# Kernel tuning notes

Measured on AMD Instinct MI355X. Metric: run time of the kernel, lower is better.

## Reference

```python
import jax, jax.numpy as jnp
import numpy as np

N_NODES = 100000


def _deg_isqrt(idx, n):
    # clamped-to-1 degree, then ^-0.5 (DGL GraphConv norm='both')
    deg = jax.ops.segment_sum(jnp.ones(idx.shape, jnp.float32), idx, num_segments=n)
    return jnp.power(jnp.maximum(deg, 1.0), -0.5)


def _graph_conv(feat, W, b, src, dst, out_isqrt, in_isqrt, n):
    # norm='both': scale by src out-degree^-1/2, mult-first (in>out), spmm, scale by dst in-degree^-1/2
    h = (feat * out_isqrt[:, None]) @ W                      # [N, out]
    h = jax.ops.segment_sum(h[src], dst, num_segments=n)     # gather/scatter over edges
    return h * in_isqrt[:, None] + b


def setup_inputs() -> dict:
    key = jax.random.key(0)
    ks = jax.random.split(key, 10)
    in_dim, h1, h2 = 512, 64, 32
    n, e = N_NODES, 800000
    features = jax.random.normal(ks[0], (n, in_dim), jnp.float32)
    src = jax.random.randint(ks[1], (e,), 0, n)
    dst = jax.random.randint(ks[2], (e,), 0, n)
    noise = jax.random.normal(ks[3], (n, h2), jnp.float32)
    s1 = 1.0 / np.sqrt(in_dim)
    s2 = 1.0 / np.sqrt(h1)
    W1 = jax.random.uniform(ks[4], (in_dim, h1), jnp.float32, -s1, s1)
    b1 = jnp.zeros((h1,), jnp.float32)
    W2 = jax.random.uniform(ks[5], (h1, h2), jnp.float32, -s2, s2)
    b2 = jnp.zeros((h2,), jnp.float32)
    W3 = jax.random.uniform(ks[6], (h1, h2), jnp.float32, -s2, s2)
    b3 = jnp.zeros((h2,), jnp.float32)
    return {"features": features, "src": src, "dst": dst, "noise": noise,
            "W1": W1, "b1": b1, "W2": W2, "b2": b2, "W3": W3, "b3": b3}


def reference(features, src, dst, noise, W1, b1, W2, b2, W3, b3):
    n = features.shape[0]
    out_isqrt = _deg_isqrt(src, n)
    in_isqrt = _deg_isqrt(dst, n)
    h = jax.nn.relu(_graph_conv(features, W1, b1, src, dst, out_isqrt, in_isqrt, n))
    mean = _graph_conv(h, W2, b2, src, dst, out_isqrt, in_isqrt, n)
    log_std = _graph_conv(h, W3, b3, src, dst, out_isqrt, in_isqrt, n)
    z = mean + noise * jnp.exp(log_std)
    return z, mean, log_std
```

## Files before the change

### kernel.cpp

```cpp
#include <hip/hip_runtime.h>
#include <hip/hip_bf16.h>


typedef __attribute__((ext_vector_type(8))) short short8;
typedef __attribute__((ext_vector_type(4))) float f32x4;
typedef unsigned short ushort_t;

static __device__ inline short f2bf(float f)
{
    union { __hip_bfloat16 h; short s; } u;
    u.h = __float2bfloat16(f);
    return u.s;
}

static __device__ inline float bf2f(ushort_t u)
{
    union { float f; unsigned v; } w;
    w.v = ((unsigned)u) << 16;
    return w.f;
}

static __device__ inline short8 cvt8(float4 lo, float4 hi)
{
    short8 r;
    r[0] = f2bf(lo.x); r[1] = f2bf(lo.y); r[2] = f2bf(lo.z); r[3] = f2bf(lo.w);
    r[4] = f2bf(hi.x); r[5] = f2bf(hi.y); r[6] = f2bf(hi.z); r[7] = f2bf(hi.w);
    return r;
}

__global__ __launch_bounds__(256) void k_setup(
    const float* __restrict__ W1, const float* __restrict__ W2,
    const float* __restrict__ W3, short* __restrict__ w1f,
    float* __restrict__ wc, int4* __restrict__ zp, int z4)
{
    int gid = blockIdx.x * 256 + threadIdx.x;
    if (gid < z4) zp[gid] = make_int4(0, 0, 0, 0);
    if (gid < 64 * 64) {
        int k = gid >> 6, c = gid & 63;
        wc[gid] = (c < 32) ? W2[k * 32 + c] : W3[k * 32 + (c - 32)];
    }
    if (gid < 512 * 64) {
        int k = gid >> 6, c = gid & 63;
        int kt = k >> 5, kk = k & 31, nt = c >> 4, lr = c & 15;
        int kg = kk >> 3, j = kk & 7;
        int l = kg * 16 + lr;
        w1f[(kt * 4 + nt) * 512 + l * 8 + j] = f2bf(W1[gid]);
    }
}

__global__ __launch_bounds__(256) void k_deg_int(
    const int* __restrict__ src, const int* __restrict__ dst,
    int* __restrict__ degS, int* __restrict__ degD, int e)
{
    int gid = blockIdx.x * 256 + threadIdx.x;
    if (gid >= e) return;
    atomicAdd(&degS[src[gid]], 1);
    atomicAdd(&degD[dst[gid]], 1);
}

__global__ __launch_bounds__(256) void k_scan_block_sums(
    const int* __restrict__ deg, int* __restrict__ partials, int n)
{
    __shared__ int red[256];
    int gid = blockIdx.x * 256 + threadIdx.x;
    red[threadIdx.x] = (gid < n) ? deg[gid] : 0;
    __syncthreads();
    for (int s = 128; s > 0; s >>= 1) {
        if (threadIdx.x < s) red[threadIdx.x] += red[threadIdx.x + s];
        __syncthreads();
    }
    if (threadIdx.x == 0) partials[blockIdx.x] = red[0];
}

__global__ __launch_bounds__(512) void k_scan_partials(
    int* __restrict__ partials, int nb)
{
    __shared__ int s[512];
    int t = threadIdx.x;
    s[t] = (t < nb) ? partials[t] : 0;
    __syncthreads();
    for (int d = 1; d < 512; d <<= 1) {
        int v = (t >= d) ? s[t - d] : 0;
        __syncthreads();
        s[t] += v;
        __syncthreads();
    }
    if (t < nb) partials[t] = (t == 0) ? 0 : s[t - 1];
}

__global__ __launch_bounds__(256) void k_scan_final(
    const int* __restrict__ degD, const int* __restrict__ degS,
    const int* __restrict__ partials,
    int* __restrict__ row_ptr, int* __restrict__ cursor,
    float* __restrict__ isq_out, float* __restrict__ isq_in, int n)
{
    __shared__ int s[256];
    int t = threadIdx.x;
    int gid = blockIdx.x * 256 + t;
    int v = (gid < n) ? degD[gid] : 0;
    s[t] = v;
    __syncthreads();
    for (int d = 1; d < 256; d <<= 1) {
        int u = (t >= d) ? s[t - d] : 0;
        __syncthreads();
        s[t] += u;
        __syncthreads();
    }
    int start = partials[blockIdx.x] + s[t] - v;
    if (gid < n) {
        row_ptr[gid] = start;
        cursor[gid]  = start;
        isq_in[gid]  = 1.0f / sqrtf((float)max(v, 1));
        isq_out[gid] = 1.0f / sqrtf((float)max(degS[gid], 1));
    }
    if (gid == n - 1) row_ptr[n] = start + v;
}

__global__ __launch_bounds__(256) void k_scatter(
    const int* __restrict__ src, const int* __restrict__ dst,
    int* __restrict__ cursor, int* __restrict__ edge_src, int e)
{
    int gid = blockIdx.x * 256 + threadIdx.x;
    if (gid >= e) return;
    int pos = atomicAdd(&cursor[dst[gid]], 1);
    edge_src[pos] = src[gid];
}

__global__ __launch_bounds__(256) void k_gemm1_mfma(
    const float* __restrict__ X, const short* __restrict__ w1f,
    const float* __restrict__ scale, ushort_t* __restrict__ Y, int n)
{
    const int tid  = threadIdx.x;
    const int l    = tid & 63;
    const int wv   = tid >> 6;
    const int row0 = (blockIdx.x * 4 + wv) * 16;
    const int lr   = l & 15;
    const int kg   = l >> 4;

    int ra = row0 + lr;  if (ra >= n) ra = n - 1;
    const float* pa = X + (size_t)ra * 512 + kg * 8;
    const short* pb = w1f + l * 8;

    f32x4 acc[4];
#pragma unroll
    for (int j = 0; j < 4; ++j) acc[j] = (f32x4){0.f, 0.f, 0.f, 0.f};

    float4 alo[4], ahi[4];
#pragma unroll
    for (int s = 0; s < 4; ++s) {
        alo[s] = *(const float4*)(pa + s * 32);
        ahi[s] = *(const float4*)(pa + s * 32 + 4);
    }
    short8 bst[2][4];
#pragma unroll
    for (int s = 0; s < 2; ++s) {
        const short* q = pb + (size_t)s * 2048;
        bst[s][0] = *(const short8*)(q);
        bst[s][1] = *(const short8*)(q + 512);
        bst[s][2] = *(const short8*)(q + 1024);
        bst[s][3] = *(const short8*)(q + 1536);
    }

#pragma unroll
    for (int kt = 0; kt < 16; ++kt) {
        short8 ca = cvt8(alo[kt & 3], ahi[kt & 3]);
        if (kt + 4 < 16) {
            const float* q = pa + (kt + 4) * 32;
            alo[kt & 3] = *(const float4*)(q);
            ahi[kt & 3] = *(const float4*)(q + 4);
        }
        short8 cb0 = bst[kt & 1][0], cb1 = bst[kt & 1][1];
        short8 cb2 = bst[kt & 1][2], cb3 = bst[kt & 1][3];
        if (kt + 2 < 16) {
            const short* q = pb + (size_t)(kt + 2) * 2048;
            bst[kt & 1][0] = *(const short8*)(q);
            bst[kt & 1][1] = *(const short8*)(q + 512);
            bst[kt & 1][2] = *(const short8*)(q + 1024);
            bst[kt & 1][3] = *(const short8*)(q + 1536);
        }
        acc[0] = __builtin_amdgcn_mfma_f32_16x16x32_bf16(ca, cb0, acc[0], 0, 0, 0);
        acc[1] = __builtin_amdgcn_mfma_f32_16x16x32_bf16(ca, cb1, acc[1], 0, 0, 0);
        acc[2] = __builtin_amdgcn_mfma_f32_16x16x32_bf16(ca, cb2, acc[2], 0, 0, 0);
        acc[3] = __builtin_amdgcn_mfma_f32_16x16x32_bf16(ca, cb3, acc[3], 0, 0, 0);
    }

#pragma unroll
    for (int m = 0; m < 4; ++m) {
        int row = row0 + kg * 4 + m;
        if (row < n) {
            float s = scale[row];
#pragma unroll
            for (int nt = 0; nt < 4; ++nt)
                Y[(size_t)row * 64 + nt * 16 + lr] =
                    (ushort_t)f2bf(acc[nt][m] * s);
        }
    }
}

__global__ __launch_bounds__(256) void k_gather_gemm2(
    const int* __restrict__ row_ptr, const int* __restrict__ edge_src,
    const ushort_t* __restrict__ x, const float* __restrict__ isq_in,
    const float* __restrict__ isq_out, const float* __restrict__ b1,
    const float* __restrict__ wc, ushort_t* __restrict__ t23, int n)
{
    __shared__ float swc[64 * 64];
    __shared__ float sh[4][64];
    const int tid = threadIdx.x;
    const int col = tid & 63;
    const int wv  = tid >> 6;

#pragma unroll
    for (int p = 0; p < 4; ++p) {
        int u = p * 256 + tid;
        *(float4*)&swc[u * 4] = *(const float4*)&wc[u * 4];
    }
    __syncthreads();

    const float bb = b1[col];

#pragma unroll 1
    for (int i = 0; i < 4; ++i) {
        int node = blockIdx.x * 16 + wv * 4 + i;
        if (node >= n) break;
        float si = isq_in[node];
        float so = isq_out[node];
        int j = row_ptr[node], jend = row_ptr[node + 1];
        float a0 = 0.f, a1 = 0.f, a2 = 0.f, a3 = 0.f;
        float a4 = 0.f, a5 = 0.f, a6 = 0.f, a7 = 0.f;
        for (; j + 7 < jend; j += 8) {
            int e0 = edge_src[j],     e1 = edge_src[j + 1];
            int e2 = edge_src[j + 2], e3 = edge_src[j + 3];
            int e4 = edge_src[j + 4], e5 = edge_src[j + 5];
            int e6 = edge_src[j + 6], e7 = edge_src[j + 7];
            a0 += bf2f(x[(size_t)e0 * 64 + col]);
            a1 += bf2f(x[(size_t)e1 * 64 + col]);
            a2 += bf2f(x[(size_t)e2 * 64 + col]);
            a3 += bf2f(x[(size_t)e3 * 64 + col]);
            a4 += bf2f(x[(size_t)e4 * 64 + col]);
            a5 += bf2f(x[(size_t)e5 * 64 + col]);
            a6 += bf2f(x[(size_t)e6 * 64 + col]);
            a7 += bf2f(x[(size_t)e7 * 64 + col]);
        }
        for (; j + 1 < jend; j += 2) {
            int e0 = edge_src[j], e1 = edge_src[j + 1];
            a0 += bf2f(x[(size_t)e0 * 64 + col]);
            a1 += bf2f(x[(size_t)e1 * 64 + col]);
        }
        if (j < jend) a2 += bf2f(x[(size_t)edge_src[j] * 64 + col]);
        float acc = ((a0 + a1) + (a2 + a3)) + ((a4 + a5) + (a6 + a7));
        float hval = fmaxf(acc * si + bb, 0.f) * so;

        sh[wv][col] = hval;
        asm volatile("s_waitcnt lgkmcnt(0)" ::: "memory");
        __builtin_amdgcn_sched_barrier(0);

        float t = 0.f;
#pragma unroll
        for (int k4 = 0; k4 < 64; k4 += 4) {
            float4 hb = *(const float4*)&sh[wv][k4];
            t += hb.x * swc[(k4 + 0) * 64 + col]
               + hb.y * swc[(k4 + 1) * 64 + col]
               + hb.z * swc[(k4 + 2) * 64 + col]
               + hb.w * swc[(k4 + 3) * 64 + col];
        }
        t23[(size_t)node * 64 + col] = (ushort_t)f2bf(t);
    }
}

__global__ __launch_bounds__(256) void k_gather_final(
    const int* __restrict__ row_ptr, const int* __restrict__ edge_src,
    const ushort_t* __restrict__ t23, const float* __restrict__ isq_in,
    const float* __restrict__ b2, const float* __restrict__ b3,
    const float* __restrict__ noise, float* __restrict__ out, int n)
{
    int lane = threadIdx.x & 63;
    int node = __builtin_amdgcn_readfirstlane(blockIdx.x * 4 + (threadIdx.x >> 6));
    if (node >= n) return;
    float si   = isq_in[node];
    float bias = (lane < 32) ? b2[lane] : b3[lane - 32];
    int total  = n * 32;
    int base   = node * 32 + (lane & 31);
    float nz   = (lane < 32) ? noise[base] : 0.f;
    int j = row_ptr[node], jend = row_ptr[node + 1];
    float a0 = 0.f, a1 = 0.f, a2 = 0.f, a3 = 0.f;
    float a4 = 0.f, a5 = 0.f, a6 = 0.f, a7 = 0.f;
    for (; j + 7 < jend; j += 8) {
        int e0 = edge_src[j],     e1 = edge_src[j + 1];
        int e2 = edge_src[j + 2], e3 = edge_src[j + 3];
        int e4 = edge_src[j + 4], e5 = edge_src[j + 5];
        int e6 = edge_src[j + 6], e7 = edge_src[j + 7];
        a0 += bf2f(t23[(size_t)e0 * 64 + lane]);
        a1 += bf2f(t23[(size_t)e1 * 64 + lane]);
        a2 += bf2f(t23[(size_t)e2 * 64 + lane]);
        a3 += bf2f(t23[(size_t)e3 * 64 + lane]);
        a4 += bf2f(t23[(size_t)e4 * 64 + lane]);
        a5 += bf2f(t23[(size_t)e5 * 64 + lane]);
        a6 += bf2f(t23[(size_t)e6 * 64 + lane]);
        a7 += bf2f(t23[(size_t)e7 * 64 + lane]);
    }
    for (; j + 1 < jend; j += 2) {
        int e0 = edge_src[j], e1 = edge_src[j + 1];
        a0 += bf2f(t23[(size_t)e0 * 64 + lane]);
        a1 += bf2f(t23[(size_t)e1 * 64 + lane]);
    }
    if (j < jend) a2 += bf2f(t23[(size_t)edge_src[j] * 64 + lane]);
    float acc = ((a0 + a1) + (a2 + a3)) + ((a4 + a5) + (a6 + a7));
    float v  = acc * si + bias;
    float lv = __shfl(v, lane | 32, 64);
    if (lane < 32) {
        float z = v + nz * expf(lv);
        out[base]         = z;
        out[total + base] = v;
    } else {
        out[2 * total + base] = v;
    }
}

extern "C" void kernel_launch(void* const* d_in, const int* in_sizes, int n_in,
                              void* d_out, int out_size, void* d_ws, size_t ws_size,
                              hipStream_t stream)
{
    const float* feat  = (const float*)d_in[0];
    const int*   src   = (const int*)d_in[1];
    const int*   dst   = (const int*)d_in[2];
    const float* noise = (const float*)d_in[3];
    const float* W1    = (const float*)d_in[4];
    const float* b1    = (const float*)d_in[5];
    const float* W2    = (const float*)d_in[6];
    const float* b2    = (const float*)d_in[7];
    const float* W3    = (const float*)d_in[8];
    const float* b3    = (const float*)d_in[9];

    const int n = in_sizes[0] / 512;
    const int e = in_sizes[1];

    float* ws      = (float*)d_ws;
    float* isq_out = ws;
    float* isq_in  = ws + n;
    float* bufA    = ws + 2 * (size_t)n;
    float* bufB    = bufA + 64 * (size_t)n;
    float* wc      = bufB + 64 * (size_t)n;
    short* w1f     = (short*)(wc + 64 * 64);
    int*   ip      = (int*)(w1f + 512 * 64);
    int* row_ptr   = ip;
    int* cursor    = ip + (n + 1);
    int* partials  = cursor + n;
    int* edge_src  = partials + 512;
    int* degS = (int*)bufA;
    int* degD = degS + n;
    float* out = (float*)d_out;

    const int nb = (n + 255) / 256;
    const int z4 = (2 * n) / 4;

    k_setup<<<(z4 + 255) / 256, 256, 0, stream>>>(
        W1, W2, W3, w1f, wc, (int4*)degS, z4);

    k_deg_int<<<(e + 255) / 256, 256, 0, stream>>>(src, dst, degS, degD, e);

    k_scan_block_sums<<<nb, 256, 0, stream>>>(degD, partials, n);
    k_scan_partials<<<1, 512, 0, stream>>>(partials, nb);
    k_scan_final<<<nb, 256, 0, stream>>>(
        degD, degS, partials, row_ptr, cursor, isq_out, isq_in, n);
    k_scatter<<<(e + 255) / 256, 256, 0, stream>>>(src, dst, cursor, edge_src, e);

    k_gemm1_mfma<<<(n + 63) / 64, 256, 0, stream>>>(
        feat, w1f, isq_out, (ushort_t*)bufA, n);

    k_gather_gemm2<<<(n + 15) / 16, 256, 0, stream>>>(
        row_ptr, edge_src, (const ushort_t*)bufA, isq_in, isq_out, b1,
        wc, (ushort_t*)bufB, n);

    k_gather_final<<<(n + 3) / 4, 256, 0, stream>>>(
        row_ptr, edge_src, (const ushort_t*)bufB, isq_in, b2, b3, noise, out, n);
}
```

Baseline: 264.7 us.

## Gather two nodes per wave and fold partial-sum scan into final scan

Removes the single-block partials scan kernel; each block of the final scan now reduces the preceding block sums itself, which drops one launch at the cost of redundant reads. Both gather kernels now process two destination nodes per wave in an interleaved loop (4-way unroll each), raising memory-level parallelism for the random row gathers and amortising the shared-memory W reads in the fused small GEMM. The final gather launches half as many blocks. Risks include load imbalance between the two nodes and higher register use.

New measurement: 315.2 us. 19.1% more time.

```diff
diff --git a/kernel.cpp b/kernel.cpp
--- a/kernel.cpp
+++ b/kernel.cpp
@@ -72,22 +72,6 @@
     if (threadIdx.x == 0) partials[blockIdx.x] = red[0];
 }
 
-__global__ __launch_bounds__(512) void k_scan_partials(
-    int* __restrict__ partials, int nb)
-{
-    __shared__ int s[512];
-    int t = threadIdx.x;
-    s[t] = (t < nb) ? partials[t] : 0;
-    __syncthreads();
-    for (int d = 1; d < 512; d <<= 1) {
-        int v = (t >= d) ? s[t - d] : 0;
-        __syncthreads();
-        s[t] += v;
-        __syncthreads();
-    }
-    if (t < nb) partials[t] = (t == 0) ? 0 : s[t - 1];
-}
-
 __global__ __launch_bounds__(256) void k_scan_final(
     const int* __restrict__ degD, const int* __restrict__ degS,
     const int* __restrict__ partials,
@@ -97,6 +81,18 @@
     __shared__ int s[256];
     int t = threadIdx.x;
     int gid = blockIdx.x * 256 + t;
+
+    int mysum = 0;
+    for (int idx = t; idx < blockIdx.x; idx += 256) mysum += partials[idx];
+    s[t] = mysum;
+    __syncthreads();
+    for (int d = 128; d > 0; d >>= 1) {
+        if (t < d) s[t] += s[t + d];
+        __syncthreads();
+    }
+    int blockBase = s[0];
+    __syncthreads();
+
     int v = (gid < n) ? degD[gid] : 0;
     s[t] = v;
     __syncthreads();
@@ -106,7 +102,7 @@
         s[t] += u;
         __syncthreads();
     }
-    int start = partials[blockIdx.x] + s[t] - v;
+    int start = blockBase + s[t] - v;
     if (gid < n) {
         row_ptr[gid] = start;
         cursor[gid]  = start;
@@ -197,6 +193,51 @@
     }
 }
 
+static __device__ inline void gather2(
+    const int* __restrict__ edge_src, const ushort_t* __restrict__ x,
+    int col, int jA, int eA, int jB, int eB, float& outA, float& outB)
+{
+    float a0 = 0.f, a1 = 0.f, a2 = 0.f, a3 = 0.f;
+    float b0 = 0.f, b1 = 0.f, b2 = 0.f, b3 = 0.f;
+    while (jA + 3 < eA && jB + 3 < eB) {
+        int ea0 = edge_src[jA],     ea1 = edge_src[jA + 1];
+        int ea2 = edge_src[jA + 2], ea3 = edge_src[jA + 3];
+        int eb0 = edge_src[jB],     eb1 = edge_src[jB + 1];
+        int eb2 = edge_src[jB + 2], eb3 = edge_src[jB + 3];
+        a0 += bf2f(x[(size_t)ea0 * 64 + col]);
+        a1 += bf2f(x[(size_t)ea1 * 64 + col]);
+        a2 += bf2f(x[(size_t)ea2 * 64 + col]);
+        a3 += bf2f(x[(size_t)ea3 * 64 + col]);
+        b0 += bf2f(x[(size_t)eb0 * 64 + col]);
+        b1 += bf2f(x[(size_t)eb1 * 64 + col]);
+        b2 += bf2f(x[(size_t)eb2 * 64 + col]);
+        b3 += bf2f(x[(size_t)eb3 * 64 + col]);
+        jA += 4; jB += 4;
+    }
+    while (jA + 3 < eA) {
+        int ea0 = edge_src[jA],     ea1 = edge_src[jA + 1];
+        int ea2 = edge_src[jA + 2], ea3 = edge_src[jA + 3];
+        a0 += bf2f(x[(size_t)ea0 * 64 + col]);
+        a1 += bf2f(x[(size_t)ea1 * 64 + col]);
+        a2 += bf2f(x[(size_t)ea2 * 64 + col]);
+        a3 += bf2f(x[(size_t)ea3 * 64 + col]);
+        jA += 4;
+    }
+    while (jB + 3 < eB) {
+        int eb0 = edge_src[jB],     eb1 = edge_src[jB + 1];
+        int eb2 = edge_src[jB + 2], eb3 = edge_src[jB + 3];
+        b0 += bf2f(x[(size_t)eb0 * 64 + col]);
+        b1 += bf2f(x[(size_t)eb1 * 64 + col]);
+        b2 += bf2f(x[(size_t)eb2 * 64 + col]);
+        b3 += bf2f(x[(size_t)eb3 * 64 + col]);
+        jB += 4;
+    }
+    for (; jA < eA; ++jA) a0 += bf2f(x[(size_t)edge_src[jA] * 64 + col]);
+    for (; jB < eB; ++jB) b0 += bf2f(x[(size_t)edge_src[jB] * 64 + col]);
+    outA = (a0 + a1) + (a2 + a3);
+    outB = (b0 + b1) + (b2 + b3);
+}
+
 __global__ __launch_bounds__(256) void k_gather_gemm2(
     const int* __restrict__ row_ptr, const int* __restrict__ edge_src,
     const ushort_t* __restrict__ x, const float* __restrict__ isq_in,
@@ -204,7 +245,7 @@
     const float* __restrict__ wc, ushort_t* __restrict__ t23, int n)
 {
     __shared__ float swc[64 * 64];
-    __shared__ float sh[4][64];
+    __shared__ float sh[4][2][64];
     const int tid = threadIdx.x;
     const int col = tid & 63;
     const int wv  = tid >> 6;
@@ -219,51 +260,41 @@
     const float bb = b1[col];
 
 #pragma unroll 1
-    for (int i = 0; i < 4; ++i) {
-        int node = blockIdx.x * 16 + wv * 4 + i;
-        if (node >= n) break;
-        float si = isq_in[node];
-        float so = isq_out[node];
-        int j = row_ptr[node], jend = row_ptr[node + 1];
-        float a0 = 0.f, a1 = 0.f, a2 = 0.f, a3 = 0.f;
-        float a4 = 0.f, a5 = 0.f, a6 = 0.f, a7 = 0.f;
-        for (; j + 7 < jend; j += 8) {
-            int e0 = edge_src[j],     e1 = edge_src[j + 1];
-            int e2 = edge_src[j + 2], e3 = edge_src[j + 3];
-            int e4 = edge_src[j + 4], e5 = edge_src[j + 5];
-            int e6 = edge_src[j + 6], e7 = edge_src[j + 7];
-            a0 += bf2f(x[(size_t)e0 * 64 + col]);
-            a1 += bf2f(x[(size_t)e1 * 64 + col]);
-            a2 += bf2f(x[(size_t)e2 * 64 + col]);
-            a3 += bf2f(x[(size_t)e3 * 64 + col]);
-            a4 += bf2f(x[(size_t)e4 * 64 + col]);
-            a5 += bf2f(x[(size_t)e5 * 64 + col]);
-            a6 += bf2f(x[(size_t)e6 * 64 + col]);
-            a7 += bf2f(x[(size_t)e7 * 64 + col]);
-        }
-        for (; j + 1 < jend; j += 2) {
-            int e0 = edge_src[j], e1 = edge_src[j + 1];
-            a0 += bf2f(x[(size_t)e0 * 64 + col]);
-            a1 += bf2f(x[(size_t)e1 * 64 + col]);
-        }
-        if (j < jend) a2 += bf2f(x[(size_t)edge_src[j] * 64 + col]);
-        float acc = ((a0 + a1) + (a2 + a3)) + ((a4 + a5) + (a6 + a7));
-        float hval = fmaxf(acc * si + bb, 0.f) * so;
-
-        sh[wv][col] = hval;
+    for (int p = 0; p < 2; ++p) {
+        int nodeA = blockIdx.x * 16 + wv * 4 + p * 2;
+        int nodeB = nodeA + 1;
+        bool vA = nodeA < n, vB = nodeB < n;
+        if (!vA) break;
+        int jA = row_ptr[nodeA], eA = row_ptr[nodeA + 1];
+        int jB = 0, eB = 0;
+        if (vB) { jB = row_ptr[nodeB]; eB = row_ptr[nodeB + 1]; }
+
+        float accA, accB;
+        gather2(edge_src, x, col, jA, eA, jB, eB, accA, accB);
+
+        float hA = fmaxf(accA * isq_in[nodeA] + bb, 0.f) * isq_out[nodeA];
+        sh[wv][0][col] = hA;
+        if (vB) {
+            float hB = fmaxf(accB * isq_in[nodeB] + bb, 0.f) * isq_out[nodeB];
+            sh[wv][1][col] = hB;
+        }
         asm volatile("s_waitcnt lgkmcnt(0)" ::: "memory");
         __builtin_amdgcn_sched_barrier(0);
 
-        float t = 0.f;
+        float tA = 0.f, tB = 0.f;
 #pragma unroll
         for (int k4 = 0; k4 < 64; k4 += 4) {
-            float4 hb = *(const float4*)&sh[wv][k4];
-            t += hb.x * swc[(k4 + 0) * 64 + col]
-               + hb.y * swc[(k4 + 1) * 64 + col]
-               + hb.z * swc[(k4 + 2) * 64 + col]
-               + hb.w * swc[(k4 + 3) * 64 + col];
-        }
-        t23[(size_t)node * 64 + col] = (ushort_t)f2bf(t);
+            float4 ha = *(const float4*)&sh[wv][0][k4];
+            float4 hb = *(const float4*)&sh[wv][1][k4];
+            float w0 = swc[(k4 + 0) * 64 + col];
+            float w1 = swc[(k4 + 1) * 64 + col];
+            float w2 = swc[(k4 + 2) * 64 + col];
+            float w3 = swc[(k4 + 3) * 64 + col];
+            tA += ha.x * w0 + ha.y * w1 + ha.z * w2 + ha.w * w3;
+            tB += hb.x * w0 + hb.y * w1 + hb.z * w2 + hb.w * w3;
+        }
+        t23[(size_t)nodeA * 64 + col] = (ushort_t)f2bf(tA);
+        if (vB) t23[(size_t)nodeB * 64 + col] = (ushort_t)f2bf(tB);
     }
 }
 
@@ -274,45 +305,51 @@
     const float* __restrict__ noise, float* __restrict__ out, int n)
 {
     int lane = threadIdx.x & 63;
-    int node = __builtin_amdgcn_readfirstlane(blockIdx.x * 4 + (threadIdx.x >> 6));
-    if (node >= n) return;
-    float si   = isq_in[node];
+    int wv   = threadIdx.x >> 6;
+    int nodeA = blockIdx.x * 8 + wv * 2;
+    int nodeB = nodeA + 1;
+    bool vA = nodeA < n, vB = nodeB < n;
+    if (!vA) return;
+
     float bias = (lane < 32) ? b2[lane] : b3[lane - 32];
     int total  = n * 32;
-    int base   = node * 32 + (lane & 31);
-    float nz   = (lane < 32) ? noise[base] : 0.f;
-    int j = row_ptr[node], jend = row_ptr[node + 1];
-    float a0 = 0.f, a1 = 0.f, a2 = 0.f, a3 = 0.f;
-    float a4 = 0.f, a5 = 0.f, a6 = 0.f, a7 = 0.f;
-    for (; j + 7 < jend; j += 8) {
-        int e0 = edge_src[j],     e1 = edge_src[j + 1];
-        int e2 = edge_src[j + 2], e3 = edge_src[j + 3];
-        int e4 = edge_src[j + 4], e5 = edge_src[j + 5];
-        int e6 = edge_src[j + 6], e7 = edge_src[j + 7];
-        a0 += bf2f(t23[(size_t)e0 * 64 + lane]);
-        a1 += bf2f(t23[(size_t)e1 * 64 + lane]);
-        a2 += bf2f(t23[(size_t)e2 * 64 + lane]);
-        a3 += bf2f(t23[(size_t)e3 * 64 + lane]);
-        a4 += bf2f(t23[(size_t)e4 * 64 + lane]);
-        a5 += bf2f(t23[(size_t)e5 * 64 + lane]);
-        a6 += bf2f(t23[(size_t)e6 * 64 + lane]);
-        a7 += bf2f(t23[(size_t)e7 * 64 + lane]);
-    }
-    for (; j + 1 < jend; j += 2) {
-        int e0 = edge_src[j], e1 = edge_src[j + 1];
-        a0 += bf2f(t23[(size_t)e0 * 64 + lane]);
-        a1 += bf2f(t23[(size_t)e1 * 64 + lane]);
-    }
-    if (j < jend) a2 += bf2f(t23[(size_t)edge_src[j] * 64 + lane]);
-    float acc = ((a0 + a1) + (a2 + a3)) + ((a4 + a5) + (a6 + a7));
-    float v  = acc * si + bias;
-    float lv = __shfl(v, lane | 32, 64);
-    if (lane < 32) {
-        float z = v + nz * expf(lv);
-        out[base]         = z;
-        out[total + base] = v;
-    } else {
-        out[2 * total + base] = v;
+    int baseA  = nodeA * 32 + (lane & 31);
+    int baseB  = nodeB * 32 + (lane & 31);
+    float siA  = isq_in[nodeA];
+    float nzA  = (lane < 32) ? noise[baseA] : 0.f;
+    float siB = 0.f, nzB = 0.f;
+    int jA = row_ptr[nodeA], eA = row_ptr[nodeA + 1];
+    int jB = 0, eB = 0;
+    if (vB) {
+        jB = row_ptr[nodeB]; eB = row_ptr[nodeB + 1];
+        siB = isq_in[nodeB];
+        nzB = (lane < 32) ? noise[baseB] : 0.f;
+    }
+
+    float accA, accB;
+    gather2(edge_src, t23, lane, jA, eA, jB, eB, accA, accB);
+
+    {
+        float v  = accA * siA + bias;
+        float lv = __shfl(v, lane | 32, 64);
+        if (lane < 32) {
+            float z = v + nzA * expf(lv);
+            out[baseA]         = z;
+            out[total + baseA] = v;
+        } else {
+            out[2 * total + baseA] = v;
+        }
+    }
+    if (vB) {
+        float v  = accB * siB + bias;
+        float lv = __shfl(v, lane | 32, 64);
+        if (lane < 32) {
+            float z = v + nzB * expf(lv);
+            out[baseB]         = z;
+            out[total + baseB] = v;
+        } else {
+            out[2 * total + baseB] = v;
+        }
     }
 }
 
@@ -359,7 +396,6 @@
     k_deg_int<<<(e + 255) / 256, 256, 0, stream>>>(src, dst, degS, degD, e);
 
     k_scan_block_sums<<<nb, 256, 0, stream>>>(degD, partials, n);
-    k_scan_partials<<<1, 512, 0, stream>>>(partials, nb);
     k_scan_final<<<nb, 256, 0, stream>>>(
         degD, degS, partials, row_ptr, cursor, isq_out, isq_in, n);
     k_scatter<<<(e + 255) / 256, 256, 0, stream>>>(src, dst, cursor, edge_src, e);
@@ -371,6 +407,6 @@
         row_ptr, edge_src, (const ushort_t*)bufA, isq_in, isq_out, b1,
         wc, (ushort_t*)bufB, n);
 
-    k_gather_final<<<(n + 3) / 4, 256, 0, stream>>>(
+    k_gather_final<<<(n + 7) / 8, 256, 0, stream>>>(
         row_ptr, edge_src, (const ushort_t*)bufB, isq_in, b2, b3, noise, out, n);
 }
```

## Merge edge scatter and GEMM1 into one launch; prefetch row metadata in gather

Applied to the files above, without the earlier changes.

The edge-scatter kernel and the first MFMA GEMM are combined into a single launch, with block index choosing which role a block plays. The two independent workloads can then overlap and one launch is saved. The layer-1 gather kernel also now loads all row pointers and degree scales for its four nodes up front, fully unrolls the per-node loop and drops a scheduling barrier. This shortens the chain of dependent loads, at the cost of more register use in the merged and unrolled code.

Measured after the change: 282.4 us. 1.07x slower.

```diff
diff --git a/kernel.cpp b/kernel.cpp
--- a/kernel.cpp
+++ b/kernel.cpp
@@ -116,24 +116,25 @@
     if (gid == n - 1) row_ptr[n] = start + v;
 }
 
-__global__ __launch_bounds__(256) void k_scatter(
+__global__ __launch_bounds__(256) void k_scatter_gemm1(
     const int* __restrict__ src, const int* __restrict__ dst,
-    int* __restrict__ cursor, int* __restrict__ edge_src, int e)
-{
-    int gid = blockIdx.x * 256 + threadIdx.x;
-    if (gid >= e) return;
-    int pos = atomicAdd(&cursor[dst[gid]], 1);
-    edge_src[pos] = src[gid];
-}
-
-__global__ __launch_bounds__(256) void k_gemm1_mfma(
+    int* __restrict__ cursor, int* __restrict__ edge_src, int e, int nsb,
     const float* __restrict__ X, const short* __restrict__ w1f,
     const float* __restrict__ scale, ushort_t* __restrict__ Y, int n)
 {
+    if (blockIdx.x < nsb) {
+        int gid = blockIdx.x * 256 + threadIdx.x;
+        if (gid >= e) return;
+        int pos = atomicAdd(&cursor[dst[gid]], 1);
+        edge_src[pos] = src[gid];
+        return;
+    }
+
+    const int bid  = blockIdx.x - nsb;
     const int tid  = threadIdx.x;
     const int l    = tid & 63;
     const int wv   = tid >> 6;
-    const int row0 = (blockIdx.x * 4 + wv) * 16;
+    const int row0 = (bid * 4 + wv) * 16;
     const int lr   = l & 15;
     const int kg   = l >> 4;
 
@@ -217,53 +218,66 @@
     __syncthreads();
 
     const float bb = b1[col];
-
-#pragma unroll 1
+    const int base = blockIdx.x * 16 + wv * 4;
+
+    int rp[5];
+#pragma unroll
+    for (int i = 0; i < 5; ++i) {
+        int idx = base + i; if (idx > n) idx = n;
+        rp[i] = row_ptr[idx];
+    }
+    float sis[4], sos[4];
+#pragma unroll
     for (int i = 0; i < 4; ++i) {
-        int node = blockIdx.x * 16 + wv * 4 + i;
-        if (node >= n) break;
-        float si = isq_in[node];
-        float so = isq_out[node];
-        int j = row_ptr[node], jend = row_ptr[node + 1];
-        float a0 = 0.f, a1 = 0.f, a2 = 0.f, a3 = 0.f;
-        float a4 = 0.f, a5 = 0.f, a6 = 0.f, a7 = 0.f;
-        for (; j + 7 < jend; j += 8) {
-            int e0 = edge_src[j],     e1 = edge_src[j + 1];
-            int e2 = edge_src[j + 2], e3 = edge_src[j + 3];
-            int e4 = edge_src[j + 4], e5 = edge_src[j + 5];
-            int e6 = edge_src[j + 6], e7 = edge_src[j + 7];
-            a0 += bf2f(x[(size_t)e0 * 64 + col]);
-            a1 += bf2f(x[(size_t)e1 * 64 + col]);
-            a2 += bf2f(x[(size_t)e2 * 64 + col]);
-            a3 += bf2f(x[(size_t)e3 * 64 + col]);
-            a4 += bf2f(x[(size_t)e4 * 64 + col]);
-            a5 += bf2f(x[(size_t)e5 * 64 + col]);
-            a6 += bf2f(x[(size_t)e6 * 64 + col]);
-            a7 += bf2f(x[(size_t)e7 * 64 + col]);
+        int idx = base + i; if (idx >= n) idx = n - 1;
+        sis[i] = isq_in[idx];
+        sos[i] = isq_out[idx];
+    }
+
+#pragma unroll
+    for (int i = 0; i < 4; ++i) {
+        int node = base + i;
+        if (node < n) {
+            int j = rp[i], jend = rp[i + 1];
+            float a0 = 0.f, a1 = 0.f, a2 = 0.f, a3 = 0.f;
+            float a4 = 0.f, a5 = 0.f, a6 = 0.f, a7 = 0.f;
+            for (; j + 7 < jend; j += 8) {
+                int e0 = edge_src[j],     e1 = edge_src[j + 1];
+                int e2 = edge_src[j + 2], e3 = edge_src[j + 3];
+                int e4 = edge_src[j + 4], e5 = edge_src[j + 5];
+                int e6 = edge_src[j + 6], e7 = edge_src[j + 7];
+                a0 += bf2f(x[(size_t)e0 * 64 + col]);
+                a1 += bf2f(x[(size_t)e1 * 64 + col]);
+                a2 += bf2f(x[(size_t)e2 * 64 + col]);
+                a3 += bf2f(x[(size_t)e3 * 64 + col]);
+                a4 += bf2f(x[(size_t)e4 * 64 + col]);
+                a5 += bf2f(x[(size_t)e5 * 64 + col]);
+                a6 += bf2f(x[(size_t)e6 * 64 + col]);
+                a7 += bf2f(x[(size_t)e7 * 64 + col]);
+            }
+            for (; j + 1 < jend; j += 2) {
+                int e0 = edge_src[j], e1 = edge_src[j + 1];
+                a0 += bf2f(x[(size_t)e0 * 64 + col]);
+                a1 += bf2f(x[(size_t)e1 * 64 + col]);
+            }
+            if (j < jend) a2 += bf2f(x[(size_t)edge_src[j] * 64 + col]);
+            float acc = ((a0 + a1) + (a2 + a3)) + ((a4 + a5) + (a6 + a7));
+            float hval = fmaxf(acc * sis[i] + bb, 0.f) * sos[i];
+
+            sh[wv][col] = hval;
+            asm volatile("s_waitcnt lgkmcnt(0)" ::: "memory");
+
+            float t = 0.f;
+#pragma unroll
+            for (int k4 = 0; k4 < 64; k4 += 4) {
+                float4 hb = *(const float4*)&sh[wv][k4];
+                t += hb.x * swc[(k4 + 0) * 64 + col]
+                   + hb.y * swc[(k4 + 1) * 64 + col]
+                   + hb.z * swc[(k4 + 2) * 64 + col]
+                   + hb.w * swc[(k4 + 3) * 64 + col];
+            }
+            t23[(size_t)node * 64 + col] = (ushort_t)f2bf(t);
         }
-        for (; j + 1 < jend; j += 2) {
-            int e0 = edge_src[j], e1 = edge_src[j + 1];
-            a0 += bf2f(x[(size_t)e0 * 64 + col]);
-            a1 += bf2f(x[(size_t)e1 * 64 + col]);
-        }
-        if (j < jend) a2 += bf2f(x[(size_t)edge_src[j] * 64 + col]);
-        float acc = ((a0 + a1) + (a2 + a3)) + ((a4 + a5) + (a6 + a7));
-        float hval = fmaxf(acc * si + bb, 0.f) * so;
-
-        sh[wv][col] = hval;
-        asm volatile("s_waitcnt lgkmcnt(0)" ::: "memory");
-        __builtin_amdgcn_sched_barrier(0);
-
-        float t = 0.f;
-#pragma unroll
-        for (int k4 = 0; k4 < 64; k4 += 4) {
-            float4 hb = *(const float4*)&sh[wv][k4];
-            t += hb.x * swc[(k4 + 0) * 64 + col]
-               + hb.y * swc[(k4 + 1) * 64 + col]
-               + hb.z * swc[(k4 + 2) * 64 + col]
-               + hb.w * swc[(k4 + 3) * 64 + col];
-        }
-        t23[(size_t)node * 64 + col] = (ushort_t)f2bf(t);
     }
 }
 
@@ -350,8 +364,10 @@
     int* degD = degS + n;
     float* out = (float*)d_out;
 
-    const int nb = (n + 255) / 256;
-    const int z4 = (2 * n) / 4;
+    const int nb  = (n + 255) / 256;
+    const int z4  = (2 * n) / 4;
+    const int nsb = (e + 255) / 256;
+    const int ngb = (n + 63) / 64;
 
     k_setup<<<(z4 + 255) / 256, 256, 0, stream>>>(
         W1, W2, W3, w1f, wc, (int4*)degS, z4);
@@ -362,9 +378,9 @@
     k_scan_partials<<<1, 512, 0, stream>>>(partials, nb);
     k_scan_final<<<nb, 256, 0, stream>>>(
         degD, degS, partials, row_ptr, cursor, isq_out, isq_in, n);
-    k_scatter<<<(e + 255) / 256, 256, 0, stream>>>(src, dst, cursor, edge_src, e);
-
-    k_gemm1_mfma<<<(n + 63) / 64, 256, 0, stream>>>(
+
+    k_scatter_gemm1<<<nsb + ngb, 256, 0, stream>>>(
+        src, dst, cursor, edge_src, e, nsb,
         feat, w1f, isq_out, (ushort_t*)bufA, n);
 
     k_gather_gemm2<<<(n + 15) / 16, 256, 0, stream>>>(
```

## Stage GEMM1 A tiles through LDS with async global_load_lds double buffering

Applied to the files above, without the earlier changes.

The first-layer GEMM kernel now loads fp32 feature rows into a double-buffered, XOR-swizzled shared-memory tile using direct global-to-LDS loads, instead of per-lane register prefetch of strided float4s. Each block cooperatively stages a 64-row by 64-column slice per step, and each wave reads its fragments from LDS. This is meant to give coalesced, asynchronous streaming of the dominant 200MB feature read and free registers. In exchange it adds a block-wide barrier per K step and 32KB of LDS per block, which may reduce occupancy.

After: 262.1 us. No clear change (-1.0%).

```diff
diff --git a/kernel.cpp b/kernel.cpp
--- a/kernel.cpp
+++ b/kernel.cpp
@@ -5,6 +5,11 @@
 typedef __attribute__((ext_vector_type(8))) short short8;
 typedef __attribute__((ext_vector_type(4))) float f32x4;
 typedef unsigned short ushort_t;
+
+#define GLOAD_LDS16(g, l)                                             \
+    __builtin_amdgcn_global_load_lds(                                 \
+        (const __attribute__((address_space(1))) void*)(g),           \
+        (__attribute__((address_space(3))) void*)(l), 16, 0, 0)
 
 static __device__ inline short f2bf(float f)
 {
@@ -130,27 +135,31 @@
     const float* __restrict__ X, const short* __restrict__ w1f,
     const float* __restrict__ scale, ushort_t* __restrict__ Y, int n)
 {
+    __shared__ float sa[2][4096];
     const int tid  = threadIdx.x;
     const int l    = tid & 63;
     const int wv   = tid >> 6;
-    const int row0 = (blockIdx.x * 4 + wv) * 16;
+    const int row0 = blockIdx.x * 64;
     const int lr   = l & 15;
     const int kg   = l >> 4;
 
-    int ra = row0 + lr;  if (ra >= n) ra = n - 1;
-    const float* pa = X + (size_t)ra * 512 + kg * 8;
+#define STAGE_A(buf, kb)                                              \
+    {                                                                 \
+        _Pragma("unroll")                                             \
+        for (int p = 0; p < 4; ++p) {                                 \
+            int u  = p * 256 + tid;                                   \
+            int r  = u >> 4;                                          \
+            int cp = u & 15;                 \
+            int rc = row0 + r; if (rc >= n) rc = n - 1;               \
+            int co = cp ^ (r & 15);       \
+            GLOAD_LDS16(X + (size_t)rc * 512 + (kb) + co * 4,         \
+                        &sa[buf][u * 4]);                             \
+        }                                                             \
+    }
+
+    STAGE_A(0, 0)
+
     const short* pb = w1f + l * 8;
-
-    f32x4 acc[4];
-#pragma unroll
-    for (int j = 0; j < 4; ++j) acc[j] = (f32x4){0.f, 0.f, 0.f, 0.f};
-
-    float4 alo[4], ahi[4];
-#pragma unroll
-    for (int s = 0; s < 4; ++s) {
-        alo[s] = *(const float4*)(pa + s * 32);
-        ahi[s] = *(const float4*)(pa + s * 32 + 4);
-    }
     short8 bst[2][4];
 #pragma unroll
     for (int s = 0; s < 2; ++s) {
@@ -161,32 +170,44 @@
         bst[s][3] = *(const short8*)(q + 1536);
     }
 
-#pragma unroll
-    for (int kt = 0; kt < 16; ++kt) {
-        short8 ca = cvt8(alo[kt & 3], ahi[kt & 3]);
-        if (kt + 4 < 16) {
-            const float* q = pa + (kt + 4) * 32;
-            alo[kt & 3] = *(const float4*)(q);
-            ahi[kt & 3] = *(const float4*)(q + 4);
-        }
-        short8 cb0 = bst[kt & 1][0], cb1 = bst[kt & 1][1];
-        short8 cb2 = bst[kt & 1][2], cb3 = bst[kt & 1][3];
-        if (kt + 2 < 16) {
-            const short* q = pb + (size_t)(kt + 2) * 2048;
-            bst[kt & 1][0] = *(const short8*)(q);
-            bst[kt & 1][1] = *(const short8*)(q + 512);
-            bst[kt & 1][2] = *(const short8*)(q + 1024);
-            bst[kt & 1][3] = *(const short8*)(q + 1536);
-        }
-        acc[0] = __builtin_amdgcn_mfma_f32_16x16x32_bf16(ca, cb0, acc[0], 0, 0, 0);
-        acc[1] = __builtin_amdgcn_mfma_f32_16x16x32_bf16(ca, cb1, acc[1], 0, 0, 0);
-        acc[2] = __builtin_amdgcn_mfma_f32_16x16x32_bf16(ca, cb2, acc[2], 0, 0, 0);
-        acc[3] = __builtin_amdgcn_mfma_f32_16x16x32_bf16(ca, cb3, acc[3], 0, 0, 0);
+    f32x4 acc[4];
+#pragma unroll
+    for (int j = 0; j < 4; ++j) acc[j] = (f32x4){0.f, 0.f, 0.f, 0.f};
+
+#pragma unroll
+    for (int s = 0; s < 8; ++s) {
+        __syncthreads();
+        if (s < 7) STAGE_A((s + 1) & 1, (s + 1) * 64)
+
+        const float* abase = &sa[s & 1][(wv * 16 + lr) * 64];
+#pragma unroll
+        for (int t = 0; t < 2; ++t) {
+            const int kt = s * 2 + t;
+            const int q0 = (t * 8 + kg * 2) ^ lr;
+            const int q1 = (t * 8 + kg * 2 + 1) ^ lr;
+            float4 vlo = *(const float4*)(abase + q0 * 4);
+            float4 vhi = *(const float4*)(abase + q1 * 4);
+            short8 ca = cvt8(vlo, vhi);
+
+            short8 cb0 = bst[kt & 1][0], cb1 = bst[kt & 1][1];
+            short8 cb2 = bst[kt & 1][2], cb3 = bst[kt & 1][3];
+            if (kt + 2 < 16) {
+                const short* qq = pb + (size_t)(kt + 2) * 2048;
+                bst[kt & 1][0] = *(const short8*)(qq);
+                bst[kt & 1][1] = *(const short8*)(qq + 512);
+                bst[kt & 1][2] = *(const short8*)(qq + 1024);
+                bst[kt & 1][3] = *(const short8*)(qq + 1536);
+            }
+            acc[0] = __builtin_amdgcn_mfma_f32_16x16x32_bf16(ca, cb0, acc[0], 0, 0, 0);
+            acc[1] = __builtin_amdgcn_mfma_f32_16x16x32_bf16(ca, cb1, acc[1], 0, 0, 0);
+            acc[2] = __builtin_amdgcn_mfma_f32_16x16x32_bf16(ca, cb2, acc[2], 0, 0, 0);
+            acc[3] = __builtin_amdgcn_mfma_f32_16x16x32_bf16(ca, cb3, acc[3], 0, 0, 0);
+        }
     }
 
 #pragma unroll
     for (int m = 0; m < 4; ++m) {
-        int row = row0 + kg * 4 + m;
+        int row = row0 + wv * 16 + kg * 4 + m;
         if (row < n) {
             float s = scale[row];
 #pragma unroll
@@ -195,6 +216,7 @@
                     (ushort_t)f2bf(acc[nt][m] * s);
         }
     }
+#undef STAGE_A
 }
 
 __global__ __launch_bounds__(256) void k_gather_gemm2(
```
